# Kernel tuning notes

Measured on AMD Instinct MI355X. Metric: run time of the kernel, lower is better.

The kernel has to match this reference:

```python
import jax, jax.numpy as jnp
import numpy as np

N_GRAPHS = 1000
P = 300                 # nodes per ring graph
N = N_GRAPHS * P        # 300000 nodes
IN_DIM = 2
HID = 128
OUT_DIM = 2


def _ring_edges():
    idx = jnp.arange(N)
    g = idx // P
    pos = idx % P
    nxt = g * P + (pos + 1) % P
    src = jnp.concatenate([idx, nxt])
    dst = jnp.concatenate([nxt, idx])
    return jnp.stack([src, dst]), g


def setup_inputs() -> dict:
    key = jax.random.key(0)
    ks = jax.random.split(key, 11)
    edge_index, batch = _ring_edges()
    x = jax.random.normal(ks[0], (N, IN_DIM), jnp.float32)

    def glorot(k, fan_in, fan_out):
        lim = np.sqrt(6.0 / (fan_in + fan_out)).astype(np.float32)
        return jax.random.uniform(k, (fan_in, fan_out), jnp.float32, -lim, lim)

    return {
        "x": x,
        "edge_index": edge_index,
        "batch": batch,
        "W1": glorot(ks[1], IN_DIM, HID), "b1": jnp.zeros((HID,), jnp.float32),
        "W2": glorot(ks[2], HID, HID),    "b2": jnp.zeros((HID,), jnp.float32),
        "W3": glorot(ks[3], HID, HID),    "b3": jnp.zeros((HID,), jnp.float32),
        "fw1": glorot(ks[4], HID, HID),   "fb1": jnp.zeros((HID,), jnp.float32),
        "fw2": glorot(ks[5], HID, OUT_DIM), "fb2": jnp.zeros((OUT_DIM,), jnp.float32),
    }


def _gcn_conv(x, W, b, src, dst, norm):
    h = x @ W                              # [N, out]
    msg = h[src] * norm[:, None]           # gather + per-edge scale
    agg = jax.ops.segment_sum(msg, dst, num_segments=N)  # scatter-add
    return agg + b


def reference(x, edge_index, batch, W1, b1, W2, b2, W3, b3, fw1, fb1, fw2, fb2):
    loop = jnp.arange(N)
    src = jnp.concatenate([edge_index[0], loop])
    dst = jnp.concatenate([edge_index[1], loop])
    deg = jax.ops.segment_sum(jnp.ones_like(dst, jnp.float32), dst, num_segments=N)
    dis = jax.lax.rsqrt(deg)               # deg >= 1 due to self-loops
    norm = dis[src] * dis[dst]             # per-edge normalization

    h = jax.nn.relu(_gcn_conv(x, W1, b1, src, dst, norm))
    h = jax.nn.relu(_gcn_conv(h, W2, b2, src, dst, norm))
    h = jax.nn.relu(_gcn_conv(h, W3, b3, src, dst, norm))

    # global mean pool per graph
    sums = jax.ops.segment_sum(h, batch, num_segments=N_GRAPHS)
    cnts = jax.ops.segment_sum(jnp.ones((N,), jnp.float32), batch, num_segments=N_GRAPHS)
    pooled = sums / cnts[:, None]

    out = jax.nn.relu(pooled @ fw1 + fb1)
    out = out @ fw2 + fb2
    return out
```

## Files before the change

kernel.cpp:

```cpp
#include <hip/hip_runtime.h>
#include <hip/hip_bf16.h>
#include <stdint.h>

#define P    300
#define HID  128
#define NG   1000
#define ARC  75
#define NTT  5

typedef __attribute__((ext_vector_type(8))) short bf16x8;
typedef __attribute__((ext_vector_type(4))) float f32x4;

__device__ short g_wsw[2 * HID * HID];
__device__ float g_pool[NG * HID];

__device__ __forceinline__ short f2bf(float f) {
    union { float f; uint32_t u; } v; v.f = f;
    uint32_t r = v.u + 0x7fffu + ((v.u >> 16) & 1u);
    return (short)(r >> 16);
}
__device__ __forceinline__ float bf2f(short s) {
    union { uint32_t u; float f; } v; v.u = ((uint32_t)(uint16_t)s) << 16;
    return v.f;
}
__device__ __forceinline__ uint32_t pkbf2(float a, float b) {
    union { __hip_bfloat162 h; uint32_t u; } cv;
    cv.h = __float22bfloat162_rn(float2{a, b});
    return cv.u;
}
__device__ __forceinline__ float unpk(int v, int ft) {
    return bf2f((short)(ft ? (((uint32_t)v) >> 16) : (v & 0xffff)));
}

__global__ __launch_bounds__(256) void k_prep(const float* __restrict__ W2,
                                              const float* __restrict__ W3) {
    int b = blockIdx.x;
    int tz = b * 256 + threadIdx.x;
    #pragma unroll
    for (int i = 0; i < 32; ++i) {
        int idx = i * 4096 + tz;
        if (idx < NG * HID) g_pool[idx] = 0.f;
    }
    const bool perm = (b < 8);
    const float* W = perm ? W2 : W3;
    short* dst = g_wsw + (perm ? 0 : HID * HID);
    int t    = (b & 7) * 256 + threadIdx.x;
    int fkey = t >> 4;
    int kc   = t & 15;
    int fsrc;
    if (perm) {
        int u = fkey >> 5, ft = (fkey >> 4) & 1, l = fkey & 15;
        fsrc = u * 32 + 2 * l + ft;
    } else fsrc = fkey;
    bf16x8 o;
    #pragma unroll
    for (int j = 0; j < 8; ++j)
        o[j] = f2bf(W[(kc * 8 + j) * HID + fsrc]);
    *(bf16x8*)&dst[(fkey * 16 + (kc ^ (fkey & 15))) * 8] = o;
}

__device__ __forceinline__ void avg_epi(const float* G, float vp0, float vn3,
                                        float b, float* o) {
    o[0] = (vp0  + G[0] + G[1]) * (1.0f / 3.0f) + b;
    o[1] = (G[0] + G[1] + G[2]) * (1.0f / 3.0f) + b;
    o[2] = (G[1] + G[2] + G[3]) * (1.0f / 3.0f) + b;
    o[3] = (G[2] + G[3] + vn3 ) * (1.0f / 3.0f) + b;
    #pragma unroll
    for (int i = 0; i < 4; ++i) o[i] = o[i] > 0.f ? o[i] : 0.f;
}

template<int POOL>
__device__ __forceinline__ void run_pass(short* __restrict__ buf,
                                         const short* __restrict__ wbase,
                                         const float* __restrict__ bias,
                                         int gidx, int tid) {
    const int lane = tid & 63, wv = tid >> 6, q = lane >> 4, lm = lane & 15;
    const int ftg0 = wv * 2;
    bf16x8 wf[2][4];
    #pragma unroll
    for (int ft = 0; ft < 2; ++ft) {
        int fkey = (ftg0 + ft) * 16 + lm;
        #pragma unroll
        for (int kk = 0; kk < 4; ++kk)
            wf[ft][kk] = *(const bf16x8*)&wbase[(fkey * 16 + ((4 * kk + q) ^ lm)) * 8];
    }
    float biaf[2];
    #pragma unroll
    for (int ft = 0; ft < 2; ++ft)
        biaf[ft] = POOL ? bias[(ftg0 + ft) * 16 + lm] : bias[wv * 32 + 2 * lm + ft];
    const int sA = (q == 0) ? (48 + lm) : (lane - 16);
    const int sB = (lane + 16) & 63;
    const int fpair = wv * 32 + 2 * lm;
    const int kcs = fpair >> 3, offs = fpair & 7;

    f32x4 G[NTT][2];
    #pragma unroll
    for (int t = 0; t < NTT; ++t) {
        G[t][0] = f32x4{0.f, 0.f, 0.f, 0.f};
        G[t][1] = f32x4{0.f, 0.f, 0.f, 0.f};
        const short* tb = buf + t * 2048;
        #pragma unroll
        for (int kk = 0; kk < 4; ++kk) {
            bf16x8 af = *(const bf16x8*)&tb[(lm * 16 + ((4 * kk + q) ^ lm)) * 8];
            G[t][0] = __builtin_amdgcn_mfma_f32_16x16x32_bf16(af, wf[0][kk], G[t][0], 0, 0, 0);
            G[t][1] = __builtin_amdgcn_mfma_f32_16x16x32_bf16(af, wf[1][kk], G[t][1], 0, 0, 0);
        }
    }
    if (!POOL) __syncthreads();

    float c15[2] = {0.f, 0.f};
    float psum[2] = {0.f, 0.f};
    #pragma unroll
    for (int t = 0; t < NTT; ++t) {
        const int tn = (t < NTT - 1) ? t + 1 : t;
        uint32_t uA = pkbf2(G[t][0][3],  G[t][1][3]);
        uint32_t uB = pkbf2(G[t][0][0],  G[t][1][0]);
        uint32_t uC = pkbf2(G[tn][0][0], G[tn][1][0]);
        int vA = __shfl((int)uA, sA, 64);
        int vB = __shfl((int)uB, sB, 64);
        int vC = __shfl((int)uC, lm, 64);
        float o2[2][4];
        #pragma unroll
        for (int ft = 0; ft < 2; ++ft) {
            float bpA = unpk(vA, ft), bpB = unpk(vB, ft), bpC = unpk(vC, ft);
            float vp0 = (q == 0) ? c15[ft] : bpA;
            float vn3 = (q == 3) ? bpC : bpB;
            avg_epi((const float*)&G[t][ft], vp0, vn3, biaf[ft], o2[ft]);
            c15[ft] = bpA;
            if (POOL) {
                #pragma unroll
                for (int i = 0; i < 4; ++i) {
                    int r = t * 16 + q * 4 + i;
                    if (r >= 2 && r <= 76) psum[ft] += o2[ft][i];
                }
            }
        }
        if (!POOL) {
            #pragma unroll
            for (int i = 0; i < 4; ++i) {
                int r = t * 16 + q * 4 + i;
                if (r >= 1 && r <= 77)
                    *(uint32_t*)&buf[(r * 16 + (kcs ^ (r & 15))) * 8 + offs] =
                        pkbf2(o2[0][i], o2[1][i]);
            }
        }
    }

    if (POOL) {
        #pragma unroll
        for (int ft = 0; ft < 2; ++ft) {
            psum[ft] += __shfl_xor(psum[ft], 16, 64);
            psum[ft] += __shfl_xor(psum[ft], 32, 64);
        }
        if (q == 0) {
            atomicAdd(&g_pool[gidx * HID + ftg0 * 16 + lm],      psum[0]);
            atomicAdd(&g_pool[gidx * HID + ftg0 * 16 + 16 + lm], psum[1]);
        }
    }
}

__global__ __launch_bounds__(256, 4) void k_graph(
        const float* __restrict__ x,
        const float* __restrict__ W1,  const float* __restrict__ b1,
        const float* __restrict__ b2v, const float* __restrict__ b3v) {
    __shared__ __align__(16) short buf[NTT * 16 * HID];
    __shared__ __align__(16) float xs[164];

    const int g   = blockIdx.x >> 2;
    const int s   = (blockIdx.x & 3) * ARC;
    const int tid = threadIdx.x;

    if (tid < 81) {
        int node = s - 3 + tid;
        node += (node < 0) ? P : 0;
        node -= (node >= P) ? P : 0;
        *(float2*)&xs[2 * tid] = *(const float2*)&x[g * 600 + node * 2];
    }
    __syncthreads();

    {
        const int kc1 = tid & 15;
        const int n0  = tid >> 4;
        float w1x[8], w1y[8], b1v[8];
        #pragma unroll
        for (int j = 0; j < 8; ++j) {
            w1x[j] = W1[kc1 * 8 + j];
            w1y[j] = W1[HID + kc1 * 8 + j];
            b1v[j] = b1[kc1 * 8 + j];
        }
        #pragma unroll
        for (int it = 0; it < NTT; ++it) {
            int r = it * 16 + n0;
            uint32_t w[4] = {0u, 0u, 0u, 0u};
            if (r < 79) {
                float2 xp = *(const float2*)&xs[2 * r];
                float2 xc = *(const float2*)&xs[2 * r + 2];
                float2 xn = *(const float2*)&xs[2 * r + 4];
                float ax = (xp.x + xc.x + xn.x) * (1.f / 3.f);
                float ay = (xp.y + xc.y + xn.y) * (1.f / 3.f);
                #pragma unroll
                for (int jj = 0; jj < 4; ++jj) {
                    float va = ax * w1x[2*jj]   + ay * w1y[2*jj]   + b1v[2*jj];
                    float vb = ax * w1x[2*jj+1] + ay * w1y[2*jj+1] + b1v[2*jj+1];
                    va = va > 0.f ? va : 0.f;
                    vb = vb > 0.f ? vb : 0.f;
                    w[jj] = pkbf2(va, vb);
                }
            }
            *(uint4*)&buf[(r * 16 + (kc1 ^ (r & 15))) * 8] =
                uint4{w[0], w[1], w[2], w[3]};
        }
    }
    __syncthreads();

    run_pass<0>(buf, g_wsw,             b2v, g, tid);
    __syncthreads();
    run_pass<1>(buf, g_wsw + HID * HID, b3v, g, tid);
}

__global__ __launch_bounds__(128) void k_fc(const float* __restrict__ fw1,
                                            const float* __restrict__ fb1,
                                            const float* __restrict__ fw2,
                                            const float* __restrict__ fb2,
                                            float* __restrict__ out) {
    int g = blockIdx.x, f = threadIdx.x;
    __shared__ float pl[128];
    __shared__ float s1[128];
    pl[f] = g_pool[g * HID + f] * (1.0f / 300.0f);
    __syncthreads();
    float o1 = fb1[f];
    #pragma unroll 8
    for (int k = 0; k < 128; ++k) o1 += pl[k] * fw1[k * 128 + f];
    s1[f] = o1 > 0.f ? o1 : 0.f;
    __syncthreads();
    {
        int o = f >> 6, ln = f & 63;
        float v = s1[ln] * fw2[ln * 2 + o] + s1[ln + 64] * fw2[(ln + 64) * 2 + o];
        #pragma unroll
        for (int off = 1; off <= 32; off <<= 1)
            v += __shfl_xor(v, off, 64);
        if (ln == 0) out[g * 2 + o] = v + fb2[o];
    }
}

extern "C" void kernel_launch(void* const* d_in, const int* in_sizes, int n_in,
                              void* d_out, int out_size, void* d_ws, size_t ws_size,
                              hipStream_t stream) {
    const float* x   = (const float*)d_in[0];
    const float* W1  = (const float*)d_in[3];
    const float* b1  = (const float*)d_in[4];
    const float* W2  = (const float*)d_in[5];
    const float* b2  = (const float*)d_in[6];
    const float* W3  = (const float*)d_in[7];
    const float* b3  = (const float*)d_in[8];
    const float* fw1 = (const float*)d_in[9];
    const float* fb1 = (const float*)d_in[10];
    const float* fw2 = (const float*)d_in[11];
    const float* fb2 = (const float*)d_in[12];
    float* out = (float*)d_out;

    k_prep <<<dim3(16),     dim3(256), 0, stream>>>(W2, W3);
    k_graph<<<dim3(NG * 4), dim3(256), 0, stream>>>(x, W1, b1, b2, b3);
    k_fc   <<<dim3(NG),     dim3(128), 0, stream>>>(fw1, fb1, fw2, fb2, out);
}
```

Measured before the change: 131.6 us.

## Process two arcs per graph block, fold bias into MFMA init, batch FC kernel

The graph kernel now launches half as many blocks, and each block loops over two arcs so its per-block setup is amortised. The bias is placed in the MFMA accumulator's initial value rather than added in the averaging epilogue. Because the neighbour values averaged with it also carry the bias, the three-way mean still yields the same result. The FC kernel now stages fw1 in shared memory (64KB), splits the K reduction over 256 threads and handles two graphs per block. The costs are fewer resident blocks for hiding latency, and a large LDS footprint in the FC kernel that limits its occupancy.

```diff
diff --git a/kernel.cpp b/kernel.cpp
--- a/kernel.cpp
+++ b/kernel.cpp
@@ -7,6 +7,7 @@
 #define NG   1000
 #define ARC  75
 #define NTT  5
+#define GRD  2000
 
 typedef __attribute__((ext_vector_type(8))) short bf16x8;
 typedef __attribute__((ext_vector_type(4))) float f32x4;
@@ -60,11 +61,12 @@
 }
 
 __device__ __forceinline__ void avg_epi(const float* G, float vp0, float vn3,
-                                        float b, float* o) {
-    o[0] = (vp0  + G[0] + G[1]) * (1.0f / 3.0f) + b;
-    o[1] = (G[0] + G[1] + G[2]) * (1.0f / 3.0f) + b;
-    o[2] = (G[1] + G[2] + G[3]) * (1.0f / 3.0f) + b;
-    o[3] = (G[2] + G[3] + vn3 ) * (1.0f / 3.0f) + b;
+                                        float* o) {
+    float s1 = G[0] + G[1], s2 = G[1] + G[2], s3 = G[2] + G[3];
+    o[0] = (vp0 + s1) * (1.0f / 3.0f);
+    o[1] = (s1 + G[2]) * (1.0f / 3.0f);
+    o[2] = (s2 + G[3]) * (1.0f / 3.0f);
+    o[3] = (s3 + vn3 ) * (1.0f / 3.0f);
     #pragma unroll
     for (int i = 0; i < 4; ++i) o[i] = o[i] > 0.f ? o[i] : 0.f;
 }
@@ -96,8 +98,8 @@
     f32x4 G[NTT][2];
     #pragma unroll
     for (int t = 0; t < NTT; ++t) {
-        G[t][0] = f32x4{0.f, 0.f, 0.f, 0.f};
-        G[t][1] = f32x4{0.f, 0.f, 0.f, 0.f};
+        G[t][0] = f32x4{biaf[0], biaf[0], biaf[0], biaf[0]};
+        G[t][1] = f32x4{biaf[1], biaf[1], biaf[1], biaf[1]};
         const short* tb = buf + t * 2048;
         #pragma unroll
         for (int kk = 0; kk < 4; ++kk) {
@@ -125,7 +127,7 @@
             float bpA = unpk(vA, ft), bpB = unpk(vB, ft), bpC = unpk(vC, ft);
             float vp0 = (q == 0) ? c15[ft] : bpA;
             float vn3 = (q == 3) ? bpC : bpB;
-            avg_epi((const float*)&G[t][ft], vp0, vn3, biaf[ft], o2[ft]);
+            avg_epi((const float*)&G[t][ft], vp0, vn3, o2[ft]);
             c15[ft] = bpA;
             if (POOL) {
                 #pragma unroll
@@ -166,80 +168,104 @@
     __shared__ __align__(16) short buf[NTT * 16 * HID];
     __shared__ __align__(16) float xs[164];
 
-    const int g   = blockIdx.x >> 2;
-    const int s   = (blockIdx.x & 3) * ARC;
     const int tid = threadIdx.x;
 
-    if (tid < 81) {
-        int node = s - 3 + tid;
-        node += (node < 0) ? P : 0;
-        node -= (node >= P) ? P : 0;
-        *(float2*)&xs[2 * tid] = *(const float2*)&x[g * 600 + node * 2];
-    }
-    __syncthreads();
-
-    {
-        const int kc1 = tid & 15;
-        const int n0  = tid >> 4;
-        float w1x[8], w1y[8], b1v[8];
-        #pragma unroll
-        for (int j = 0; j < 8; ++j) {
-            w1x[j] = W1[kc1 * 8 + j];
-            w1y[j] = W1[HID + kc1 * 8 + j];
-            b1v[j] = b1[kc1 * 8 + j];
-        }
-        #pragma unroll
-        for (int it = 0; it < NTT; ++it) {
-            int r = it * 16 + n0;
-            uint32_t w[4] = {0u, 0u, 0u, 0u};
-            if (r < 79) {
-                float2 xp = *(const float2*)&xs[2 * r];
-                float2 xc = *(const float2*)&xs[2 * r + 2];
-                float2 xn = *(const float2*)&xs[2 * r + 4];
-                float ax = (xp.x + xc.x + xn.x) * (1.f / 3.f);
-                float ay = (xp.y + xc.y + xn.y) * (1.f / 3.f);
-                #pragma unroll
-                for (int jj = 0; jj < 4; ++jj) {
-                    float va = ax * w1x[2*jj]   + ay * w1y[2*jj]   + b1v[2*jj];
-                    float vb = ax * w1x[2*jj+1] + ay * w1y[2*jj+1] + b1v[2*jj+1];
-                    va = va > 0.f ? va : 0.f;
-                    vb = vb > 0.f ? vb : 0.f;
-                    w[jj] = pkbf2(va, vb);
+    for (int rep = 0; rep < 2; ++rep) {
+        const int arc = blockIdx.x + rep * GRD;
+        const int g   = arc >> 2;
+        const int s   = (arc & 3) * ARC;
+
+        if (tid < 81) {
+            int node = s - 3 + tid;
+            node += (node < 0) ? P : 0;
+            node -= (node >= P) ? P : 0;
+            *(float2*)&xs[2 * tid] = *(const float2*)&x[g * 600 + node * 2];
+        }
+        __syncthreads();
+
+        {
+            const int kc1 = tid & 15;
+            const int n0  = tid >> 4;
+            float w1x[8], w1y[8], b1v[8];
+            #pragma unroll
+            for (int j = 0; j < 8; ++j) {
+                w1x[j] = W1[kc1 * 8 + j];
+                w1y[j] = W1[HID + kc1 * 8 + j];
+                b1v[j] = b1[kc1 * 8 + j];
+            }
+            #pragma unroll
+            for (int it = 0; it < NTT; ++it) {
+                int r = it * 16 + n0;
+                uint32_t w[4] = {0u, 0u, 0u, 0u};
+                if (r < 79) {
+                    float2 xp = *(const float2*)&xs[2 * r];
+                    float2 xc = *(const float2*)&xs[2 * r + 2];
+                    float2 xn = *(const float2*)&xs[2 * r + 4];
+                    float ax = (xp.x + xc.x + xn.x) * (1.f / 3.f);
+                    float ay = (xp.y + xc.y + xn.y) * (1.f / 3.f);
+                    #pragma unroll
+                    for (int jj = 0; jj < 4; ++jj) {
+                        float va = ax * w1x[2*jj]   + ay * w1y[2*jj]   + b1v[2*jj];
+                        float vb = ax * w1x[2*jj+1] + ay * w1y[2*jj+1] + b1v[2*jj+1];
+                        va = va > 0.f ? va : 0.f;
+                        vb = vb > 0.f ? vb : 0.f;
+                        w[jj] = pkbf2(va, vb);
+                    }
                 }
-            }
-            *(uint4*)&buf[(r * 16 + (kc1 ^ (r & 15))) * 8] =
-                uint4{w[0], w[1], w[2], w[3]};
-        }
-    }
-    __syncthreads();
-
-    run_pass<0>(buf, g_wsw,             b2v, g, tid);
-    __syncthreads();
-    run_pass<1>(buf, g_wsw + HID * HID, b3v, g, tid);
-}
-
-__global__ __launch_bounds__(128) void k_fc(const float* __restrict__ fw1,
+                *(uint4*)&buf[(r * 16 + (kc1 ^ (r & 15))) * 8] =
+                    uint4{w[0], w[1], w[2], w[3]};
+            }
+        }
+        __syncthreads();
+
+        run_pass<0>(buf, g_wsw,             b2v, g, tid);
+        __syncthreads();
+        run_pass<1>(buf, g_wsw + HID * HID, b3v, g, tid);
+    }
+}
+
+__global__ __launch_bounds__(256) void k_fc(const float* __restrict__ fw1,
                                             const float* __restrict__ fb1,
                                             const float* __restrict__ fw2,
                                             const float* __restrict__ fb2,
                                             float* __restrict__ out) {
-    int g = blockIdx.x, f = threadIdx.x;
-    __shared__ float pl[128];
-    __shared__ float s1[128];
-    pl[f] = g_pool[g * HID + f] * (1.0f / 300.0f);
-    __syncthreads();
-    float o1 = fb1[f];
-    #pragma unroll 8
-    for (int k = 0; k < 128; ++k) o1 += pl[k] * fw1[k * 128 + f];
-    s1[f] = o1 > 0.f ? o1 : 0.f;
-    __syncthreads();
-    {
-        int o = f >> 6, ln = f & 63;
-        float v = s1[ln] * fw2[ln * 2 + o] + s1[ln + 64] * fw2[(ln + 64) * 2 + o];
-        #pragma unroll
-        for (int off = 1; off <= 32; off <<= 1)
-            v += __shfl_xor(v, off, 64);
-        if (ln == 0) out[g * 2 + o] = v + fb2[o];
+    __shared__ float w1s[HID * HID];
+    __shared__ float pl[128], parts[256], s1[128];
+    const int tid = threadIdx.x;
+
+    #pragma unroll
+    for (int i = 0; i < 16; ++i) {
+        int t = i * 256 + tid;
+        *(float4*)&w1s[t * 4] = *(const float4*)&fw1[t * 4];
+    }
+
+    for (int rep = 0; rep < 2; ++rep) {
+        int g = blockIdx.x * 2 + rep;
+        __syncthreads();
+        if (tid < 128) pl[tid] = g_pool[g * HID + tid] * (1.0f / 300.0f);
+        __syncthreads();
+        {
+            int f = tid & 127, half = tid >> 7;
+            float p = 0.f;
+            #pragma unroll 8
+            for (int k = half * 64; k < half * 64 + 64; ++k)
+                p += pl[k] * w1s[k * 128 + f];
+            parts[half * 128 + f] = p;
+        }
+        __syncthreads();
+        if (tid < 128) {
+            float o1 = fb1[tid] + parts[tid] + parts[128 + tid];
+            s1[tid] = o1 > 0.f ? o1 : 0.f;
+        }
+        __syncthreads();
+        if (tid < 128) {
+            int o = tid >> 6, ln = tid & 63;
+            float v = s1[ln] * fw2[ln * 2 + o] + s1[ln + 64] * fw2[(ln + 64) * 2 + o];
+            #pragma unroll
+            for (int off = 1; off <= 32; off <<= 1)
+                v += __shfl_xor(v, off, 64);
+            if (ln == 0) out[g * 2 + o] = v + fb2[o];
+        }
     }
 }
 
@@ -259,7 +285,7 @@
     const float* fb2 = (const float*)d_in[12];
     float* out = (float*)d_out;
 
-    k_prep <<<dim3(16),     dim3(256), 0, stream>>>(W2, W3);
-    k_graph<<<dim3(NG * 4), dim3(256), 0, stream>>>(x, W1, b1, b2, b3);
-    k_fc   <<<dim3(NG),     dim3(128), 0, stream>>>(fw1, fb1, fw2, fb2, out);
-}
+    k_prep <<<dim3(16),  dim3(256), 0, stream>>>(W2, W3);
+    k_graph<<<dim3(GRD), dim3(256), 0, stream>>>(x, W1, b1, b2, b3);
+    k_fc   <<<dim3(500), dim3(256), 0, stream>>>(fw1, fb1, fw2, fb2, out);
+}
```

Measured after the change: 188.0 us. 1.43x slower.
